# Kernel tuning notes

Hardware: AMD Instinct MI355X
Metric: run time of the kernel (lower is better)

Reference implementation:

```python
import jax, jax.numpy as jnp
import numpy as np

B, N, D_ROI = 16, 128, 12544   # images, detections/image, C*roi*roi = 256*7*7
HID, PARTS = 128, 22
DTH, CTH = 50.0, 0.8           # dist / cosine thresholds
EPS = 1e-12


def setup_inputs() -> dict:
    key = jax.random.key(0)
    ks = jax.random.split(key, 6)
    d_in = D_ROI + 2
    fv = jax.random.normal(ks[0], (B, N, D_ROI), jnp.float32)
    ctr = jax.random.uniform(ks[1], (B, N, 2), jnp.float32) * 640.0  # xyxyn*640 centers
    W1 = jax.random.normal(ks[2], (d_in, HID), jnp.float32) / np.float32(np.sqrt(d_in))
    b1 = jnp.zeros((HID,), jnp.float32)
    W2 = jax.random.normal(ks[3], (HID, HID), jnp.float32) / np.float32(np.sqrt(HID))
    b2 = jnp.zeros((HID,), jnp.float32)
    Wc = jax.random.normal(ks[4], (HID, PARTS), jnp.float32) / np.float32(np.sqrt(HID))
    bc = jnp.zeros((PARTS,), jnp.float32)
    return {"fv": fv, "ctr": ctr, "W1": W1, "b1": b1, "W2": W2, "b2": b2, "Wc": Wc, "bc": bc}


def _adjacency(fv, ctr):
    """Per-image graph build: (cdist < dth) | (cosine > cth), + PyG self-loop."""
    # squared pairwise distance (compare against DTH^2; avoids sqrt at 0)
    d2 = jnp.sum((ctr[:, :, None, :] - ctr[:, None, :, :]) ** 2, axis=-1)  # [B,N,N]
    fvn = fv / jnp.maximum(jnp.linalg.norm(fv, axis=-1, keepdims=True), EPS)
    cos = jnp.einsum("bnd,bmd->bnm", fvn, fvn)                              # [B,N,N]
    A = ((d2 < DTH * DTH) | (cos > CTH)).astype(jnp.float32)
    # GCNConv(add_self_loops=True) adds weight-1 self loops on top of existing edges
    A = A + jnp.eye(N, dtype=jnp.float32)
    deg = jnp.sum(A, axis=-1)                                               # >= 2 on diag
    dinv = jax.lax.rsqrt(deg)
    return dinv[:, :, None] * A * dinv[:, None, :]                          # D^-1/2 A D^-1/2


def reference(fv, ctr, W1, b1, W2, b2, Wc, bc):
    A_hat = _adjacency(fv, ctr)                         # [B,N,N]
    x = jnp.concatenate([fv, ctr], axis=-1)             # [B,N,D_roi+2]
    h = jax.nn.relu(jnp.einsum("bnm,bmh->bnh", A_hat, x @ W1) + b1)
    h = jax.nn.relu(jnp.einsum("bnm,bmh->bnh", A_hat, h @ W2) + b2)
    hg = jnp.mean(h, axis=1)                            # global_mean_pool per image
    logits = hg @ Wc + bc                               # [B, PARTS]
    return logits
```

## Files before the change

### kernel.cpp

```cpp
#include <hip/hip_runtime.h>
#include <stdint.h>

#define DROI   12544
#define BIMG   16
#define NDET   128
#define NHID   128

typedef __bf16 bf16x8 __attribute__((ext_vector_type(8)));
typedef float  f32x4  __attribute__((ext_vector_type(4)));

__device__ __forceinline__ unsigned pk2(float a, float b){
  unsigned ua = __float_as_uint(a), ub = __float_as_uint(b);
  ua = (ua + 0x7fffu + ((ua >> 16) & 1u)) >> 16;
  ub = (ub + 0x7fffu + ((ub >> 16) & 1u)) >> 16;
  return ua | (ub << 16);
}
__device__ __forceinline__ unsigned short bf1(float a){
  unsigned ua = __float_as_uint(a);
  return (unsigned short)((ua + 0x7fffu + ((ua >> 16) & 1u)) >> 16);
}
__device__ __forceinline__ f32x4 mfma16(bf16x8 a, bf16x8 b, f32x4 c){
  return __builtin_amdgcn_mfma_f32_16x16x32_bf16(a, b, c, 0, 0, 0);
}
__device__ __forceinline__ void gl_lds16(const void* g, void* l){
  __builtin_amdgcn_global_load_lds(
      (const __attribute__((address_space(1))) unsigned int*)g,
      (__attribute__((address_space(3))) unsigned int*)l, 16, 0, 0);
}
__device__ __forceinline__ bf16x8 ldfrag128(const short* base, int row, int bo){
  const char* p = (const char*)base + row * 128 + (bo ^ ((row & 7) << 4));
  return *(const bf16x8*)p;
}
__device__ __forceinline__ bf16x8 ldfrag256(const short* base, int row, int bo){
  const char* p = (const char*)base + row * 256 + (bo ^ ((row & 7) << 4));
  return *(const bf16x8*)p;
}

__global__ __launch_bounds__(256) void k0_wt(const float* __restrict__ W1,
                                             unsigned short* __restrict__ Wt){
  __shared__ float tile[64][133];
  const int t  = threadIdx.x;
  const int k0 = blockIdx.x * 64;
  const int r0 = t >> 5;
  const int c4 = (t & 31) * 4;
#pragma unroll
  for (int i = 0; i < 8; ++i){
    int r = r0 + i * 8;
    float4 v = *(const float4*)(W1 + (long)(k0 + r) * NHID + c4);
    tile[r][c4+0] = v.x; tile[r][c4+1] = v.y; tile[r][c4+2] = v.z; tile[r][c4+3] = v.w;
  }
  __syncthreads();
  const int h  = t >> 1;
  const int kc = (t & 1) * 32;
  unsigned* dst = (unsigned*)(Wt + (long)h * DROI + k0 + kc);
#pragma unroll
  for (int kk = 0; kk < 32; kk += 2)
    dst[kk >> 1] = pk2(tile[kc + kk][h], tile[kc + kk + 1][h]);
}

template<int SK>
__global__ __launch_bounds__(512, 4) void k1_main(const float* __restrict__ fv,
    const unsigned short* __restrict__ Wt, unsigned* __restrict__ part){
  constexpr int KC = DROI / SK;
  constexpr int NT = KC / 64;
  __shared__ __align__(16) short lsA[2][8192];
  __shared__ __align__(16) short lsB[2][8192];
  const int tid  = threadIdx.x;
  const int wave = tid >> 6, lane = tid & 63;
  const int s = blockIdx.x, b = blockIdx.y;
  const int kbase = s * KC;

  f32x4 acc[2][8];
  {
    f32x4 z = {0.f, 0.f, 0.f, 0.f};
#pragma unroll
    for (int m = 0; m < 2; ++m)
#pragma unroll
      for (int c = 0; c < 8; ++c) acc[m][c] = z;
  }

  const int r0   = tid >> 2;
  const int colf = (tid & 3) * 16;
  const float* fvt = fv + (long)(b * NDET + r0) * DROI + kbase + colf;
  const int hh  = lane >> 3;
  const int seg = (lane & 7) ^ hh;

  float4 stg[4];
#pragma unroll
  for (int j = 0; j < 2; ++j){
    int call = wave * 2 + j;
    int h = call * 8 + hh;
    const char* g = (const char*)Wt + (long)h * (DROI * 2) + (long)kbase * 2 + seg * 16;
    gl_lds16(g, (char*)lsB[0] + call * 1024);
  }
#pragma unroll
  for (int i = 0; i < 4; ++i) stg[i] = *(const float4*)(fvt + i * 4);
  {
    char* basep = (char*)lsA[0];
    uint4 w0, w1;
    w0.x = pk2(stg[0].x, stg[0].y); w0.y = pk2(stg[0].z, stg[0].w);
    w0.z = pk2(stg[1].x, stg[1].y); w0.w = pk2(stg[1].z, stg[1].w);
    w1.x = pk2(stg[2].x, stg[2].y); w1.y = pk2(stg[2].z, stg[2].w);
    w1.z = pk2(stg[3].x, stg[3].y); w1.w = pk2(stg[3].z, stg[3].w);
    const int bo = colf * 2, sw = (r0 & 7) << 4;
    *(uint4*)(basep + r0 * 128 + (bo ^ sw)) = w0;
    *(uint4*)(basep + r0 * 128 + ((bo + 16) ^ sw)) = w1;
  }
  __syncthreads();

  const int outw = wave >> 2;
  const int mq   = wave & 3;
  const int lq   = lane & 15;
  int buf = 0;
  for (int t = 0; t < NT; ++t){
    const int nt = t + 1;
    if (nt < NT){
#pragma unroll
      for (int j = 0; j < 2; ++j){
        int call = wave * 2 + j;
        int h = call * 8 + hh;
        const char* g = (const char*)Wt + (long)h * (DROI * 2)
                      + (long)(kbase + nt * 64) * 2 + seg * 16;
        gl_lds16(g, (char*)lsB[buf ^ 1] + call * 1024);
      }
      const float* fp = fvt + nt * 64;
#pragma unroll
      for (int i = 0; i < 4; ++i) stg[i] = *(const float4*)(fp + i * 4);
    }
    const short* A  = lsA[buf];
    const short* Bs = outw ? lsB[buf] : lsA[buf];
#pragma unroll
    for (int kk = 0; kk < 2; ++kk){
      const int bo = kk * 64 + (lane >> 4) * 16;
      bf16x8 a0 = ldfrag128(A, mq * 32 + lq, bo);
      bf16x8 a1 = ldfrag128(A, mq * 32 + 16 + lq, bo);
#pragma unroll
      for (int cb = 0; cb < 8; ++cb){
        bf16x8 bb = ldfrag128(Bs, cb * 16 + lq, bo);
        acc[0][cb] = mfma16(a0, bb, acc[0][cb]);
        acc[1][cb] = mfma16(a1, bb, acc[1][cb]);
      }
    }
    if (nt < NT){
      char* basep = (char*)lsA[buf ^ 1];
      uint4 w0, w1;
      w0.x = pk2(stg[0].x, stg[0].y); w0.y = pk2(stg[0].z, stg[0].w);
      w0.z = pk2(stg[1].x, stg[1].y); w0.w = pk2(stg[1].z, stg[1].w);
      w1.x = pk2(stg[2].x, stg[2].y); w1.y = pk2(stg[2].z, stg[2].w);
      w1.z = pk2(stg[3].x, stg[3].y); w1.w = pk2(stg[3].z, stg[3].w);
      const int bo = colf * 2, sw = (r0 & 7) << 4;
      *(uint4*)(basep + r0 * 128 + (bo ^ sw)) = w0;
      *(uint4*)(basep + r0 * 128 + ((bo + 16) ^ sw)) = w1;
    }
    __syncthreads();
    buf ^= 1;
  }

  const int slot = mq * 64 + lane;
  uint4* dst4 = (uint4*)(part + (((long)s * 32 + b * 2 + outw) * 8192));
#pragma unroll
  for (int g = 0; g < 8; ++g){
    const int m = g >> 2, cb0 = (g & 3) * 2;
    uint4 w;
    w.x = pk2(acc[m][cb0][0],     acc[m][cb0][1]);
    w.y = pk2(acc[m][cb0][2],     acc[m][cb0][3]);
    w.z = pk2(acc[m][cb0 + 1][0], acc[m][cb0 + 1][1]);
    w.w = pk2(acc[m][cb0 + 1][2], acc[m][cb0 + 1][3]);
    dst4[g * 256 + slot] = w;
  }
}

template<int SK>
__global__ __launch_bounds__(256) void k_reduce(const unsigned* __restrict__ part,
                                                float* __restrict__ fin){
  const int gq   = blockIdx.x * 256 + threadIdx.x;
  const int q    = gq & 8191;
  const int bo2  = gq >> 13;
  float lo = 0.f, hi = 0.f;
#pragma unroll
  for (int s = 0; s < SK; ++s){
    unsigned v = part[(long)s * 262144 + (long)bo2 * 8192 + q];
    lo += __uint_as_float(v << 16);
    hi += __uint_as_float(v & 0xffff0000u);
  }
  const int g    = q >> 10;
  const int slot = (q & 1023) >> 2;
  const int w    = q & 3;
  const int m  = g >> 2;
  const int cb = (g & 3) * 2 + (w >> 1);
  const int ip = w & 1;
  const int mq = slot >> 6, lane = slot & 63;
  const int R = mq * 32 + m * 16 + (lane >> 4) * 4 + ip * 2;
  const int C = cb * 16 + (lane & 15);
  float* f = fin + (long)bo2 * 16384;
  if ((bo2 & 1) == 0){
    f[R * 128 + C] = lo;
    f[(R + 1) * 128 + C] = hi;
  } else {
    float2 v2; v2.x = lo; v2.y = hi;
    *(float2*)(f + C * 128 + R) = v2;
  }
}

__global__ __launch_bounds__(256, 1) void k2f(const float* __restrict__ fin,
    const float* __restrict__ ctr, const float* __restrict__ W1,
    const float* __restrict__ b1, const float* __restrict__ W2,
    const float* __restrict__ b2, const float* __restrict__ Wc,
    const float* __restrict__ bc, float* __restrict__ out){
  __shared__ __align__(16) short Ah[16384];
  __shared__ __align__(16) short Bu[16384];
  __shared__ __align__(16) short Cu[16384];
  __shared__ float sm2[256];
  __shared__ float sctr[256];
  const int b   = blockIdx.x;
  const int tid = threadIdx.x;
  const float* G  = fin + (long)b * 32768;
  const float* Yt = G + 16384;

  sctr[tid] = ctr[b * 256 + tid];
  if (tid < 128){
    float g = G[tid * 129];
    sm2[tid] = 1.0f / fmaxf(sqrtf(g), 1e-12f);
  }
  __syncthreads();

  const int   i   = tid >> 1;
  const int   jb  = (tid & 1) * 64;
  const float invni = sm2[i];
  const float cxi = sctr[2 * i], cyi = sctr[2 * i + 1];
  unsigned m0 = 0, m1 = 0;
  int degloc = 0;
  for (int j4 = 0; j4 < 64; j4 += 4){
    float4 g4 = *(const float4*)(G + i * 128 + jb + j4);
    float gg[4] = {g4.x, g4.y, g4.z, g4.w};
#pragma unroll
    for (int u = 0; u < 4; ++u){
      int j = jb + j4 + u;
      float cs = gg[u] * invni * sm2[j];
      float dx = cxi - sctr[2 * j];
      float dy = cyi - sctr[2 * j + 1];
      float d2 = dx * dx + dy * dy;
      if (d2 < 2500.0f || cs > 0.8f){
        int bp = j4 + u;
        if (bp < 32) m0 |= (1u << bp); else m1 |= (1u << (bp - 32));
        ++degloc;
      }
    }
  }
  if (i >= jb && i < jb + 64) ++degloc;
  int degfull = degloc + __shfl_xor(degloc, 1);
  if ((tid & 1) == 0) sm2[128 + i] = rsqrtf((float)degfull);
  __syncthreads();

  {
    const float dinvi = sm2[128 + i];
    char* AhB = (char*)Ah;
    for (int jp = 0; jp < 64; jp += 2){
      int j0 = jb + jp, j1 = j0 + 1;
      float a0 = (((jp   < 32) ? ((m0 >> jp)       & 1u) : ((m1 >> (jp - 32))     & 1u)) ? 1.f : 0.f);
      float a1 = (((jp+1 < 32) ? ((m0 >> (jp + 1)) & 1u) : ((m1 >> (jp + 1 - 32)) & 1u)) ? 1.f : 0.f);
      if (i == j0) a0 += 1.f;
      if (i == j1) a1 += 1.f;
      float v0 = dinvi * a0 * sm2[128 + j0];
      float v1 = dinvi * a1 * sm2[128 + j1];
      int bo = j0 * 2;
      *(unsigned*)(AhB + i * 256 + (bo ^ ((i & 7) << 4))) = pk2(v0, v1);
    }
  }

  {
    const int c     = tid & 127;
    const int khalf = tid >> 7;
    char* WB = (char*)Cu;
    for (int k8 = khalf * 64; k8 < khalf * 64 + 64; k8 += 8){
      float f[8];
#pragma unroll
      for (int u = 0; u < 8; ++u) f[u] = W2[(k8 + u) * 128 + c];
      uint4 w;
      w.x = pk2(f[0], f[1]); w.y = pk2(f[2], f[3]);
      w.z = pk2(f[4], f[5]); w.w = pk2(f[6], f[7]);
      int bo = k8 * 2;
      *(uint4*)(WB + c * 256 + (bo ^ ((c & 7) << 4))) = w;
    }
  }
  {
    const int cr = tid >> 1;
    const int kh = (tid & 1) * 64;
    const float w1a = W1[(long)12544 * NHID + cr];
    const float w1b = W1[(long)12545 * NHID + cr];
    const float* Yr = Yt + cr * 128 + kh;
    char* YtB = (char*)Bu;
    for (int k8 = 0; k8 < 64; k8 += 8){
      float4 va = *(const float4*)(Yr + k8);
      float4 vb = *(const float4*)(Yr + k8 + 4);
      float f[8] = {va.x, va.y, va.z, va.w, vb.x, vb.y, vb.z, vb.w};
#pragma unroll
      for (int u = 0; u < 8; ++u){
        int k = kh + k8 + u;
        f[u] += sctr[2 * k] * w1a + sctr[2 * k + 1] * w1b;
      }
      uint4 w;
      w.x = pk2(f[0], f[1]); w.y = pk2(f[2], f[3]);
      w.z = pk2(f[4], f[5]); w.w = pk2(f[6], f[7]);
      int bo = (kh + k8) * 2;
      *(uint4*)(YtB + cr * 256 + (bo ^ ((cr & 7) << 4))) = w;
    }
  }
  __syncthreads();

  const int wave = tid >> 6, lane = tid & 63;
  const int lq = lane & 15;
  f32x4 acc[2][8];
  f32x4 z4 = {0.f, 0.f, 0.f, 0.f};

#pragma unroll
  for (int r = 0; r < 2; ++r)
#pragma unroll
    for (int cc = 0; cc < 8; ++cc) acc[r][cc] = z4;
#pragma unroll
  for (int ks = 0; ks < 4; ++ks){
    const int bo = ks * 64 + (lane >> 4) * 16;
    bf16x8 a0 = ldfrag256(Ah, (wave*2+0)*16 + lq, bo);
    bf16x8 a1 = ldfrag256(Ah, (wave*2+1)*16 + lq, bo);
#pragma unroll
    for (int cb = 0; cb < 8; ++cb){
      bf16x8 bb = ldfrag256(Bu, cb*16 + lq, bo);
      acc[0][cb] = mfma16(a0, bb, acc[0][cb]);
      acc[1][cb] = mfma16(a1, bb, acc[1][cb]);
    }
  }
  __syncthreads();
  {
    char* BuB = (char*)Bu;
#pragma unroll
    for (int rb = 0; rb < 2; ++rb){
      const int R0 = wave*32 + rb*16 + (lane >> 4)*4;
#pragma unroll
      for (int cb = 0; cb < 8; ++cb){
        const int C = cb*16 + lq;
        const float bb1 = b1[C];
#pragma unroll
        for (int u = 0; u < 4; ++u){
          float v = fmaxf(acc[rb][cb][u] + bb1, 0.f);
          int row = R0 + u;
          *(unsigned short*)(BuB + row * 256 + ((C * 2) ^ ((row & 7) << 4))) = bf1(v);
        }
      }
    }
  }
  __syncthreads();

#pragma unroll
  for (int r = 0; r < 2; ++r)
#pragma unroll
    for (int cc = 0; cc < 8; ++cc) acc[r][cc] = z4;
#pragma unroll
  for (int ks = 0; ks < 4; ++ks){
    const int bo = ks * 64 + (lane >> 4) * 16;
    bf16x8 a0 = ldfrag256(Bu, (wave*2+0)*16 + lq, bo);
    bf16x8 a1 = ldfrag256(Bu, (wave*2+1)*16 + lq, bo);
#pragma unroll
    for (int cb = 0; cb < 8; ++cb){
      bf16x8 bb = ldfrag256(Cu, cb*16 + lq, bo);
      acc[0][cb] = mfma16(a0, bb, acc[0][cb]);
      acc[1][cb] = mfma16(a1, bb, acc[1][cb]);
    }
  }
  __syncthreads();
  {
    char* BuB = (char*)Bu;
#pragma unroll
    for (int rb = 0; rb < 2; ++rb){
      const int R0 = wave*32 + rb*16 + (lane >> 4)*4;
#pragma unroll
      for (int cb = 0; cb < 8; ++cb){
        const int C = cb*16 + lq;
#pragma unroll
        for (int u = 0; u < 4; ++u){
          int k = R0 + u;
          *(unsigned short*)(BuB + C * 256 + ((k * 2) ^ ((C & 7) << 4))) = bf1(acc[rb][cb][u]);
        }
      }
    }
  }
  __syncthreads();

#pragma unroll
  for (int r = 0; r < 2; ++r)
#pragma unroll
    for (int cc = 0; cc < 8; ++cc) acc[r][cc] = z4;
#pragma unroll
  for (int ks = 0; ks < 4; ++ks){
    const int bo = ks * 64 + (lane >> 4) * 16;
    bf16x8 a0 = ldfrag256(Ah, (wave*2+0)*16 + lq, bo);
    bf16x8 a1 = ldfrag256(Ah, (wave*2+1)*16 + lq, bo);
#pragma unroll
    for (int cb = 0; cb < 8; ++cb){
      bf16x8 bb = ldfrag256(Bu, cb*16 + lq, bo);
      acc[0][cb] = mfma16(a0, bb, acc[0][cb]);
      acc[1][cb] = mfma16(a1, bb, acc[1][cb]);
    }
  }
  float colp[8];
#pragma unroll
  for (int cb = 0; cb < 8; ++cb){
    const int C = cb*16 + lq;
    const float bb2 = b2[C];
    float sum = 0.f;
#pragma unroll
    for (int rb = 0; rb < 2; ++rb)
#pragma unroll
      for (int u = 0; u < 4; ++u)
        sum += fmaxf(acc[rb][cb][u] + bb2, 0.f);
    colp[cb] = sum;
  }
#pragma unroll
  for (int cb = 0; cb < 8; ++cb){
    float v = colp[cb];
    v += __shfl_xor(v, 16);
    v += __shfl_xor(v, 32);
    colp[cb] = v;
  }
  __syncthreads();
  float* hgp = (float*)Cu;
  if ((lane >> 4) == 0){
#pragma unroll
    for (int cb = 0; cb < 8; ++cb)
      hgp[wave * 128 + cb * 16 + lane] = colp[cb];
  }
  __syncthreads();
  float* hg = hgp + 512;
  if (tid < 128)
    hg[tid] = (hgp[tid] + hgp[128 + tid] + hgp[256 + tid] + hgp[384 + tid]) * (1.0f / 128.0f);
  __syncthreads();
  if (tid < 22){
    float a2 = bc[tid];
    for (int h = 0; h < 128; ++h) a2 += hg[h] * Wc[h * 22 + tid];
    out[b * 22 + tid] = a2;
  }
}

extern "C" void kernel_launch(void* const* d_in, const int* in_sizes, int n_in,
                              void* d_out, int out_size, void* d_ws, size_t ws_size,
                              hipStream_t stream){
  (void)in_sizes; (void)n_in; (void)out_size;
  const float* fv  = (const float*)d_in[0];
  const float* ctr = (const float*)d_in[1];
  const float* W1  = (const float*)d_in[2];
  const float* b1  = (const float*)d_in[3];
  const float* W2  = (const float*)d_in[4];
  const float* b2  = (const float*)d_in[5];
  const float* Wc  = (const float*)d_in[6];
  const float* bc  = (const float*)d_in[7];
  char* ws = (char*)d_ws;
  float* out = (float*)d_out;

  const unsigned long SZ_WT  = (unsigned long)NHID * DROI * 2;
  const unsigned long SZ_FIN = (unsigned long)BIMG * 2 * 16384 * 4;

  const unsigned long need28 = SZ_WT + 28UL * 1048576UL + SZ_FIN;
  const bool big = (ws_size >= need28);
  const int SK = big ? 28 : 14;

  unsigned short* Wt   = (unsigned short*)(ws);
  unsigned*       part = (unsigned*)(ws + SZ_WT);
  float*          fin  = (float*)(ws + SZ_WT + (unsigned long)SK * 1048576UL);

  k0_wt<<<dim3(DROI / 64), dim3(256), 0, stream>>>(W1, Wt);
  if (big){
    k1_main<28><<<dim3(28, BIMG), dim3(512), 0, stream>>>(fv, Wt, part);
    k_reduce<28><<<dim3(1024), dim3(256), 0, stream>>>(part, fin);
  } else {
    k1_main<14><<<dim3(14, BIMG), dim3(512), 0, stream>>>(fv, Wt, part);
    k_reduce<14><<<dim3(1024), dim3(256), 0, stream>>>(part, fin);
  }
  k2f<<<dim3(BIMG), dim3(256), 0, stream>>>(fin, ctr, W1, b1, W2, b2, Wc, bc, out);
}
```

Baseline: 65.35 us.

## Triple-buffer W1 tiles, remap workgroups across XCDs, and coalesce reduce stores

Result: faster. 62.16 us (-4.9%).

```diff
diff --git a/kernel.cpp b/kernel.cpp
--- a/kernel.cpp
+++ b/kernel.cpp
@@ -63,11 +63,18 @@
     const unsigned short* __restrict__ Wt, unsigned* __restrict__ part){
   constexpr int KC = DROI / SK;
   constexpr int NT = KC / 64;
+  static_assert(NT >= 3, "pipeline needs >=3 tiles");
   __shared__ __align__(16) short lsA[2][8192];
-  __shared__ __align__(16) short lsB[2][8192];
+  __shared__ __align__(16) short lsB[3][8192];
   const int tid  = threadIdx.x;
   const int wave = tid >> 6, lane = tid & 63;
-  const int s = blockIdx.x, b = blockIdx.y;
+
+  const int nwg  = SK * BIMG;
+  const int cpx  = nwg >> 3;
+  const int orig = blockIdx.x;
+  const int wg   = (orig & 7) * cpx + (orig >> 3);
+  const int s = wg >> 4;
+  const int b = wg & 15;
   const int kbase = s * KC;
 
   f32x4 acc[2][8];
@@ -80,80 +87,85 @@
   }
 
   const int r0   = tid >> 2;
-  const int colf = (tid & 3) * 16;
+  const int colf = (tid & 3) * 4;
+  const int sw   = (r0 & 7) << 4;
   const float* fvt = fv + (long)(b * NDET + r0) * DROI + kbase + colf;
   const int hh  = lane >> 3;
   const int seg = (lane & 7) ^ hh;
 
-  float4 stg[4];
-#pragma unroll
-  for (int j = 0; j < 2; ++j){
-    int call = wave * 2 + j;
-    int h = call * 8 + hh;
-    const char* g = (const char*)Wt + (long)h * (DROI * 2) + (long)kbase * 2 + seg * 16;
-    gl_lds16(g, (char*)lsB[0] + call * 1024);
-  }
-#pragma unroll
-  for (int i = 0; i < 4; ++i) stg[i] = *(const float4*)(fvt + i * 4);
-  {
-    char* basep = (char*)lsA[0];
-    uint4 w0, w1;
-    w0.x = pk2(stg[0].x, stg[0].y); w0.y = pk2(stg[0].z, stg[0].w);
-    w0.z = pk2(stg[1].x, stg[1].y); w0.w = pk2(stg[1].z, stg[1].w);
-    w1.x = pk2(stg[2].x, stg[2].y); w1.y = pk2(stg[2].z, stg[2].w);
-    w1.z = pk2(stg[3].x, stg[3].y); w1.w = pk2(stg[3].z, stg[3].w);
-    const int bo = colf * 2, sw = (r0 & 7) << 4;
-    *(uint4*)(basep + r0 * 128 + (bo ^ sw)) = w0;
-    *(uint4*)(basep + r0 * 128 + ((bo + 16) ^ sw)) = w1;
-  }
-  __syncthreads();
-
   const int outw = wave >> 2;
   const int mq   = wave & 3;
   const int lq   = lane & 15;
-  int buf = 0;
+
+  float4 stg[4];
+
+  auto issueF = [&](int t){
+    const float* fp = fvt + t * 64;
+#pragma unroll
+    for (int i = 0; i < 4; ++i) stg[i] = *(const float4*)(fp + i * 16);
+  };
+  auto issueG = [&](int t, int bufi){
+#pragma unroll
+    for (int j = 0; j < 2; ++j){
+      int call = wave * 2 + j;
+      int h = call * 8 + hh;
+      const char* g = (const char*)Wt + (long)h * (DROI * 2)
+                    + (long)(kbase + t * 64) * 2 + seg * 16;
+      gl_lds16(g, (char*)lsB[bufi] + call * 1024);
+    }
+  };
+  auto writeA = [&](int abuf){
+    char* basep = (char*)lsA[abuf];
+#pragma unroll
+    for (int i = 0; i < 4; ++i){
+      uint2 w; w.x = pk2(stg[i].x, stg[i].y); w.y = pk2(stg[i].z, stg[i].w);
+      int bo = (colf + i * 16) * 2;
+      *(uint2*)(basep + r0 * 128 + (bo ^ sw)) = w;
+    }
+  };
+
+  issueF(0);
+  __builtin_amdgcn_sched_barrier(0);
+  issueG(0, 0);
+  issueG(1, 1);
+  __builtin_amdgcn_sched_barrier(0);
+  writeA(0);
+  asm volatile("s_waitcnt vmcnt(2)" ::: "memory");
+  asm volatile("s_waitcnt lgkmcnt(0)" ::: "memory");
+  __builtin_amdgcn_sched_barrier(0);
+  __builtin_amdgcn_s_barrier();
+  __builtin_amdgcn_sched_barrier(0);
+
+#pragma unroll
   for (int t = 0; t < NT; ++t){
-    const int nt = t + 1;
-    if (nt < NT){
-#pragma unroll
-      for (int j = 0; j < 2; ++j){
-        int call = wave * 2 + j;
-        int h = call * 8 + hh;
-        const char* g = (const char*)Wt + (long)h * (DROI * 2)
-                      + (long)(kbase + nt * 64) * 2 + seg * 16;
-        gl_lds16(g, (char*)lsB[buf ^ 1] + call * 1024);
+    if (t + 1 < NT) issueF(t + 1);
+    __builtin_amdgcn_sched_barrier(0);
+    if (t + 2 < NT) issueG(t + 2, (t + 2) % 3);
+    __builtin_amdgcn_sched_barrier(0);
+    {
+      const short* A  = lsA[t & 1];
+      const short* Bs = outw ? lsB[t % 3] : lsA[t & 1];
+#pragma unroll
+      for (int kk = 0; kk < 2; ++kk){
+        const int bo = kk * 64 + (lane >> 4) * 16;
+        bf16x8 a0 = ldfrag128(A, mq * 32 + lq, bo);
+        bf16x8 a1 = ldfrag128(A, mq * 32 + 16 + lq, bo);
+#pragma unroll
+        for (int cb = 0; cb < 8; ++cb){
+          bf16x8 bb = ldfrag128(Bs, cb * 16 + lq, bo);
+          acc[0][cb] = mfma16(a0, bb, acc[0][cb]);
+          acc[1][cb] = mfma16(a1, bb, acc[1][cb]);
+        }
       }
-      const float* fp = fvt + nt * 64;
-#pragma unroll
-      for (int i = 0; i < 4; ++i) stg[i] = *(const float4*)(fp + i * 4);
-    }
-    const short* A  = lsA[buf];
-    const short* Bs = outw ? lsB[buf] : lsA[buf];
-#pragma unroll
-    for (int kk = 0; kk < 2; ++kk){
-      const int bo = kk * 64 + (lane >> 4) * 16;
-      bf16x8 a0 = ldfrag128(A, mq * 32 + lq, bo);
-      bf16x8 a1 = ldfrag128(A, mq * 32 + 16 + lq, bo);
-#pragma unroll
-      for (int cb = 0; cb < 8; ++cb){
-        bf16x8 bb = ldfrag128(Bs, cb * 16 + lq, bo);
-        acc[0][cb] = mfma16(a0, bb, acc[0][cb]);
-        acc[1][cb] = mfma16(a1, bb, acc[1][cb]);
-      }
-    }
-    if (nt < NT){
-      char* basep = (char*)lsA[buf ^ 1];
-      uint4 w0, w1;
-      w0.x = pk2(stg[0].x, stg[0].y); w0.y = pk2(stg[0].z, stg[0].w);
-      w0.z = pk2(stg[1].x, stg[1].y); w0.w = pk2(stg[1].z, stg[1].w);
-      w1.x = pk2(stg[2].x, stg[2].y); w1.y = pk2(stg[2].z, stg[2].w);
-      w1.z = pk2(stg[3].x, stg[3].y); w1.w = pk2(stg[3].z, stg[3].w);
-      const int bo = colf * 2, sw = (r0 & 7) << 4;
-      *(uint4*)(basep + r0 * 128 + (bo ^ sw)) = w0;
-      *(uint4*)(basep + r0 * 128 + ((bo + 16) ^ sw)) = w1;
-    }
-    __syncthreads();
-    buf ^= 1;
+    }
+    __builtin_amdgcn_sched_barrier(0);
+    if (t + 1 < NT){
+      writeA((t + 1) & 1);
+      asm volatile("s_waitcnt lgkmcnt(0)" ::: "memory");
+      __builtin_amdgcn_sched_barrier(0);
+      __builtin_amdgcn_s_barrier();
+      __builtin_amdgcn_sched_barrier(0);
+    }
   }
 
   const int slot = mq * 64 + lane;
@@ -173,13 +185,16 @@
 template<int SK>
 __global__ __launch_bounds__(256) void k_reduce(const unsigned* __restrict__ part,
                                                 float* __restrict__ fin){
-  const int gq   = blockIdx.x * 256 + threadIdx.x;
-  const int q    = gq & 8191;
-  const int bo2  = gq >> 13;
+  __shared__ float tile[16][33];
+  const int tid = threadIdx.x;
+  const int B   = blockIdx.x;
+  const int bo2 = B >> 5;
+  const int q   = (B & 31) * 256 + tid;
   float lo = 0.f, hi = 0.f;
+  const unsigned* p = part + (long)bo2 * 8192 + q;
 #pragma unroll
   for (int s = 0; s < SK; ++s){
-    unsigned v = part[(long)s * 262144 + (long)bo2 * 8192 + q];
+    unsigned v = p[(long)s * 262144];
     lo += __uint_as_float(v << 16);
     hi += __uint_as_float(v & 0xffff0000u);
   }
@@ -187,18 +202,31 @@
   const int slot = (q & 1023) >> 2;
   const int w    = q & 3;
   const int m  = g >> 2;
-  const int cb = (g & 3) * 2 + (w >> 1);
+  const int cb1 = w >> 1;
   const int ip = w & 1;
   const int mq = slot >> 6, lane = slot & 63;
-  const int R = mq * 32 + m * 16 + (lane >> 4) * 4 + ip * 2;
-  const int C = cb * 16 + (lane & 15);
+  const int r   = ((lane >> 4) << 2) + (ip << 1);
+  const int col = (cb1 << 4) + (lane & 15);
+  tile[r][col]     = lo;
+  tile[r + 1][col] = hi;
+  __syncthreads();
+  const int Rbase = mq * 32 + m * 16;
+  const int Cbase = (g & 3) * 32;
   float* f = fin + (long)bo2 * 16384;
   if ((bo2 & 1) == 0){
-    f[R * 128 + C] = lo;
-    f[(R + 1) * 128 + C] = hi;
+#pragma unroll
+    for (int k = 0; k < 2; ++k){
+      int idx = k * 256 + tid;
+      int rr = idx >> 5, cc = idx & 31;
+      f[(Rbase + rr) * 128 + Cbase + cc] = tile[rr][cc];
+    }
   } else {
-    float2 v2; v2.x = lo; v2.y = hi;
-    *(float2*)(f + C * 128 + R) = v2;
+#pragma unroll
+    for (int k = 0; k < 2; ++k){
+      int idx = k * 256 + tid;
+      int cc = idx >> 4, rr = idx & 15;
+      f[(Cbase + cc) * 128 + Rbase + rr] = tile[rr][cc];
+    }
   }
 }
 
@@ -468,10 +496,10 @@
 
   k0_wt<<<dim3(DROI / 64), dim3(256), 0, stream>>>(W1, Wt);
   if (big){
-    k1_main<28><<<dim3(28, BIMG), dim3(512), 0, stream>>>(fv, Wt, part);
+    k1_main<28><<<dim3(28 * BIMG), dim3(512), 0, stream>>>(fv, Wt, part);
     k_reduce<28><<<dim3(1024), dim3(256), 0, stream>>>(part, fin);
   } else {
-    k1_main<14><<<dim3(14, BIMG), dim3(512), 0, stream>>>(fv, Wt, part);
+    k1_main<14><<<dim3(14 * BIMG), dim3(512), 0, stream>>>(fv, Wt, part);
     k_reduce<14><<<dim3(1024), dim3(256), 0, stream>>>(part, fin);
   }
   k2f<<<dim3(BIMG), dim3(256), 0, stream>>>(fin, ctr, W1, b1, W2, b2, Wc, bc, out);
```
